# Performance work log

Measured on AMD Instinct MI355X. Metric: run time of the kernel, lower is better.

Reference implementation:

```python
import jax, jax.numpy as jnp
import numpy as np

NUM_LAYER = 5
EMB = 300
BN_EPS = 1e-5
NUM_BOND_TYPE = 6
NUM_BOND_DIR = 3
SELF_LOOP_TYPE = 4  # pretrain-gnns self-loop edge attr = [4, 0]


def setup_inputs() -> dict:
    key = jax.random.key(0)
    ks = jax.random.split(key, 12)
    N, E, D = 100000, 250000, EMB
    x = jax.random.normal(ks[0], (N, D), dtype=jnp.float32)
    edge_index = jax.random.randint(ks[1], (2, E), 0, N, dtype=jnp.int64)
    edge_attr = jax.random.randint(ks[2], (E, 2), 0, 3, dtype=jnp.int64)
    L = NUM_LAYER
    W1 = jax.random.normal(ks[3], (L, D, 2 * D), dtype=jnp.float32) * 0.05
    b1 = jnp.zeros((L, 2 * D), dtype=jnp.float32)
    W2 = jax.random.normal(ks[4], (L, 2 * D, D), dtype=jnp.float32) * 0.05
    b2 = jnp.zeros((L, D), dtype=jnp.float32)
    E1 = jax.random.normal(ks[5], (L, NUM_BOND_TYPE, D), dtype=jnp.float32) * 0.05
    E2 = jax.random.normal(ks[6], (L, NUM_BOND_DIR, D), dtype=jnp.float32) * 0.05
    gamma = jnp.ones((L, D), dtype=jnp.float32)
    beta = jnp.zeros((L, D), dtype=jnp.float32)
    return {"x": x, "edge_index": edge_index, "edge_attr": edge_attr,
            "W1": W1, "b1": b1, "W2": W2, "b2": b2,
            "E1": E1, "E2": E2, "gamma": gamma, "beta": beta}


def reference(x, edge_index, edge_attr, W1, b1, W2, b2, E1, E2, gamma, beta):
    N = x.shape[0]
    src, dst = edge_index[0], edge_index[1]
    bt, bd = edge_attr[:, 0], edge_attr[:, 1]
    h = x
    for l in range(NUM_LAYER):
        # GINEConv: message = x_j + edge_embedding, aggr='add', with self loops
        edge_emb = E1[l][bt] + E2[l][bd]                 # [E, D]
        self_emb = E1[l][SELF_LOOP_TYPE] + E2[l][0]      # [D]
        msg = h[src] + edge_emb                          # [E, D] gather
        agg = jax.ops.segment_sum(msg, dst, num_segments=N) + h + self_emb
        # update MLP: Linear(D,2D) -> ReLU -> Linear(2D,D)
        m = jax.nn.relu(agg @ W1[l] + b1[l]) @ W2[l] + b2[l]
        # BatchNorm1d in training mode (batch stats over nodes, biased var)
        mu = m.mean(axis=0)
        var = m.var(axis=0)
        m = (m - mu) * jax.lax.rsqrt(var + BN_EPS) * gamma[l] + beta[l]
        if l < NUM_LAYER - 1:  # ReLU on all but last layer; dropout ratio 0 -> no-op
            m = jax.nn.relu(m)
        h = m
    return h  # JK == 'last'
```

## Files before the change

kernel.cpp:

```cpp
#include <hip/hip_runtime.h>
#include <hip/hip_bf16.h>

#define NN 100000
#define NE 250000
#define DD 300
#define DDB 304
#define NL 5
#define MPAD 100096
#define KA1 320
#define N1 608
#define N1T 640
#define K2 608
#define N2T 384
#define NBLK 391
#define NCMB 19

typedef __attribute__((ext_vector_type(8))) short short8;
typedef __attribute__((ext_vector_type(4))) float f32x4;

#define GLBP(x) ((const __attribute__((address_space(1))) unsigned int*)(x))
#define LDSP(x) ((__attribute__((address_space(3))) unsigned int*)(x))
#define WAITV(N) asm volatile("s_waitcnt vmcnt(" #N ")" ::: "memory")

__device__ __forceinline__ ushort f2bf(float f){
  unsigned u = __float_as_uint(f);
  u += 0x7FFFu + ((u >> 16) & 1u);
  return (ushort)(u >> 16);
}
__device__ __forceinline__ float bf2f(ushort h){
  return __uint_as_float((unsigned)h << 16);
}
__device__ __forceinline__ unsigned pk2(float a, float b){
  return (unsigned)f2bf(a) | ((unsigned)f2bf(b) << 16);
}

__global__ void prep_weights(const float* __restrict__ W1, const float* __restrict__ W2,
                             ushort* __restrict__ W1T, ushort* __restrict__ W2T){
  int idx = blockIdx.x * 256 + threadIdx.x;
  const int total1 = NL * N1T * KA1;
  const int total2 = NL * N2T * K2;
  if (idx < total1){
    int l = idx / (N1T * KA1);
    int rem = idx % (N1T * KA1);
    int n = rem / KA1, k = rem % KA1;
    float v = (n < 2*DD && k < DD) ? W1[(size_t)l*DD*2*DD + (size_t)k*2*DD + n] : 0.0f;
    W1T[idx] = f2bf(v);
  } else {
    int idx2 = idx - total1;
    if (idx2 < total2){
      int l = idx2 / (N2T * K2);
      int rem = idx2 % (N2T * K2);
      int n = rem / K2, k = rem % K2;
      float v = (n < DD && k < 2*DD) ? W2[(size_t)l*2*DD*DD + (size_t)k*DD + n] : 0.0f;
      W2T[idx2] = f2bf(v);
    }
  }
}

__global__ void prep_ctab(const float* __restrict__ E1, const float* __restrict__ E2,
                          float* __restrict__ ctab){
  int idx = blockIdx.x * 256 + threadIdx.x;
  if (idx >= NL * NCMB * DDB) return;
  int l = idx / (NCMB * DDB);
  int rem = idx % (NCMB * DDB);
  int c = rem / DDB, d = rem % DDB;
  float v = 0.0f;
  if (d < DD){
    int bt = (c < 18) ? (c / 3) : 4;
    int bd = (c < 18) ? (c % 3) : 0;
    v = E1[(size_t)l*6*DD + bt*DD + d] + E2[(size_t)l*3*DD + bd*DD + d];
  }
  ctab[idx] = v;
}

__global__ void csr_count(const int* __restrict__ ei, int* __restrict__ deg){
  int e = blockIdx.x * 256 + threadIdx.x;
  if (e < NE) atomicAdd(&deg[ei[NE + e]], 1);
}

__global__ void scan_blk(const int* __restrict__ deg, int* __restrict__ rs, int* __restrict__ bsum){
  __shared__ int tmp[256];
  int i = blockIdx.x * 256 + threadIdx.x;
  int v = (i < NN) ? deg[i] : 0;
  tmp[threadIdx.x] = v;
  __syncthreads();
  #pragma unroll
  for (int off = 1; off < 256; off <<= 1){
    int t = (threadIdx.x >= off) ? tmp[threadIdx.x - off] : 0;
    __syncthreads();
    tmp[threadIdx.x] += t;
    __syncthreads();
  }
  if (i < NN) rs[i] = tmp[threadIdx.x] - v;
  if (threadIdx.x == 255) bsum[blockIdx.x] = tmp[255];
}

__global__ void scan_top(int* __restrict__ bsum){
  __shared__ int tmp[512];
  int v = (threadIdx.x < NBLK) ? bsum[threadIdx.x] : 0;
  tmp[threadIdx.x] = v;
  __syncthreads();
  #pragma unroll
  for (int off = 1; off < 512; off <<= 1){
    int t = (threadIdx.x >= off) ? tmp[threadIdx.x - off] : 0;
    __syncthreads();
    tmp[threadIdx.x] += t;
    __syncthreads();
  }
  if (threadIdx.x < NBLK) bsum[threadIdx.x] = tmp[threadIdx.x] - v;
}

__global__ void scan_add(int* __restrict__ rs, const int* __restrict__ bsum){
  int i = blockIdx.x * 256 + threadIdx.x;
  if (i < NN) rs[i] += bsum[blockIdx.x];
  if (i == 0) rs[NN] = NE;
}

__global__ void csr_fill(const int* __restrict__ ei, const int* __restrict__ ea,
                         const int* __restrict__ rs, int* __restrict__ cursor,
                         int* __restrict__ edges){
  int e = blockIdx.x * 256 + threadIdx.x;
  if (e < NE){
    int dst = ei[NE + e];
    int src = ei[e];
    int c = ea[2*e] * 3 + ea[2*e + 1];
    int p = rs[dst] + atomicAdd(&cursor[dst], 1);
    edges[p] = src | (c << 20);
  }
}

template<int HBF>
__global__ __launch_bounds__(256) void gather_agg(
    const void* __restrict__ hp, const float2* __restrict__ ss,
    const float* __restrict__ ctab_l,
    const int* __restrict__ rs, const int* __restrict__ edges,
    ushort* __restrict__ agg)
{
  int lane = threadIdx.x & 63;
  int wq = __builtin_amdgcn_readfirstlane(threadIdx.x >> 6);
  int wid = blockIdx.x * 4 + wq;
  int nw = gridDim.x * 4;
  int dA = lane * 4;
  int dB = 256 + lane * 4;
  bool laneB  = (lane < 16);
  bool validB = (dB < DD);

  float scA[4], shA[4], scB[4], shB[4];
  if (HBF){
    #pragma unroll
    for (int j = 0; j < 4; ++j){
      float2 s = ss[dA + j]; scA[j] = s.x; shA[j] = s.y;
    }
    if (validB){
      #pragma unroll
      for (int j = 0; j < 4; ++j){
        float2 s = ss[dB + j]; scB[j] = s.x; shB[j] = s.y;
      }
    }
  }

  const float*  hf = (const float*)hp;
  const ushort* hb = (const ushort*)hp;
  const float* ctS = ctab_l + 18*DDB;

  for (int row = wid; row < MPAD; row += nw){
    float a0=0,a1=0,a2=0,a3=0, b0=0,b1=0,b2=0,b3=0;
    if (row < NN){
      if (HBF){
        uint2 hw = *(const uint2*)(hb + (size_t)row*DDB + dA);
        a0 = fmaxf(bf2f((ushort)hw.x)*scA[0]+shA[0],0.f)      + ctS[dA+0];
        a1 = fmaxf(bf2f((ushort)(hw.x>>16))*scA[1]+shA[1],0.f)+ ctS[dA+1];
        a2 = fmaxf(bf2f((ushort)hw.y)*scA[2]+shA[2],0.f)      + ctS[dA+2];
        a3 = fmaxf(bf2f((ushort)(hw.y>>16))*scA[3]+shA[3],0.f)+ ctS[dA+3];
        if (validB){
          uint2 hv = *(const uint2*)(hb + (size_t)row*DDB + dB);
          b0 = fmaxf(bf2f((ushort)hv.x)*scB[0]+shB[0],0.f)      + ctS[dB+0];
          b1 = fmaxf(bf2f((ushort)(hv.x>>16))*scB[1]+shB[1],0.f)+ ctS[dB+1];
          b2 = fmaxf(bf2f((ushort)hv.y)*scB[2]+shB[2],0.f)      + ctS[dB+2];
          b3 = fmaxf(bf2f((ushort)(hv.y>>16))*scB[3]+shB[3],0.f)+ ctS[dB+3];
        }
      } else {
        float4 hv = *(const float4*)(hf + (size_t)row*DD + dA);
        a0 = hv.x + ctS[dA+0]; a1 = hv.y + ctS[dA+1];
        a2 = hv.z + ctS[dA+2]; a3 = hv.w + ctS[dA+3];
        if (validB){
          float4 hv2 = *(const float4*)(hf + (size_t)row*DD + dB);
          b0 = hv2.x + ctS[dB+0]; b1 = hv2.y + ctS[dB+1];
          b2 = hv2.z + ctS[dB+2]; b3 = hv2.w + ctS[dB+3];
        }
      }
      int p = rs[row], pe = rs[row + 1];
      for (; p < pe; ++p){
        int ew = edges[p];
        int src = ew & 0xFFFFF;
        const float* ct = ctab_l + (ew >> 20)*DDB;
        if (HBF){
          uint2 hw = *(const uint2*)(hb + (size_t)src*DDB + dA);
          a0 += fmaxf(bf2f((ushort)hw.x)*scA[0]+shA[0],0.f)      + ct[dA+0];
          a1 += fmaxf(bf2f((ushort)(hw.x>>16))*scA[1]+shA[1],0.f)+ ct[dA+1];
          a2 += fmaxf(bf2f((ushort)hw.y)*scA[2]+shA[2],0.f)      + ct[dA+2];
          a3 += fmaxf(bf2f((ushort)(hw.y>>16))*scA[3]+shA[3],0.f)+ ct[dA+3];
          if (validB){
            uint2 hv = *(const uint2*)(hb + (size_t)src*DDB + dB);
            b0 += fmaxf(bf2f((ushort)hv.x)*scB[0]+shB[0],0.f)      + ct[dB+0];
            b1 += fmaxf(bf2f((ushort)(hv.x>>16))*scB[1]+shB[1],0.f)+ ct[dB+1];
            b2 += fmaxf(bf2f((ushort)hv.y)*scB[2]+shB[2],0.f)      + ct[dB+2];
            b3 += fmaxf(bf2f((ushort)(hv.y>>16))*scB[3]+shB[3],0.f)+ ct[dB+3];
          }
        } else {
          float4 hv = *(const float4*)(hf + (size_t)src*DD + dA);
          a0 += hv.x + ct[dA+0]; a1 += hv.y + ct[dA+1];
          a2 += hv.z + ct[dA+2]; a3 += hv.w + ct[dA+3];
          if (validB){
            float4 hv2 = *(const float4*)(hf + (size_t)src*DD + dB);
            b0 += hv2.x + ct[dB+0]; b1 += hv2.y + ct[dB+1];
            b2 += hv2.z + ct[dB+2]; b3 += hv2.w + ct[dB+3];
          }
        }
      }
    }
    ushort* ag = agg + (size_t)row*KA1;
    uint2 oA; oA.x = pk2(a0, a1); oA.y = pk2(a2, a3);
    *(uint2*)(ag + dA) = oA;
    if (laneB){
      uint2 oB;
      if (validB){ oB.x = pk2(b0, b1); oB.y = pk2(b2, b3); }
      else       { oB.x = 0; oB.y = 0; }
      *(uint2*)(ag + dB) = oB;
    }
  }
}

template<int OUT_BF16, int RELU, int STATS>
__global__ __launch_bounds__(256) void gemm_128(
    const ushort* __restrict__ A, int lda,
    const ushort* __restrict__ B, int ldb,
    void* __restrict__ Cp, int ldc,
    int kTiles, const float* __restrict__ bias, int biasN,
    int Mvalid, int Nvalid, int nColTiles, float* __restrict__ statf)
{
  __shared__ ushort As[5][4096];
  __shared__ ushort Bs[5][4096];
  int tid = threadIdx.x;
  int lane = tid & 63, w = tid >> 6;
  int wm = (w >> 1) * 64, wn = (w & 1) * 64;

  int nwg = gridDim.x;
  int q = nwg >> 3, r = nwg & 7;
  int xcd = blockIdx.x & 7, idx = blockIdx.x >> 3;
  int bid = (xcd < r ? xcd * (q + 1) : r * (q + 1) + (xcd - r) * q) + idx;
  int m0 = (bid / nColTiles) * 128;
  int n0 = (bid % nColTiles) * 128;

  int r0 = tid >> 2;
  int kc = ((tid & 3) ^ ((tid >> 3) & 3)) * 8;
  const ushort* Ap = A + (size_t)(m0 + r0)*lda + kc;
  const ushort* Bp = B + (size_t)(n0 + r0)*ldb + kc;

  f32x4 acc[4][4] = {};

#define STAGE(buf, kt) do { \
    int _ko = (kt) * 32; \
    __builtin_amdgcn_global_load_lds(GLBP(Ap + _ko),                  LDSP(&As[buf][w*512]),        16, 0, 0); \
    __builtin_amdgcn_global_load_lds(GLBP(Ap + _ko + (size_t)64*lda), LDSP(&As[buf][w*512 + 2048]), 16, 0, 0); \
    __builtin_amdgcn_global_load_lds(GLBP(Bp + _ko),                  LDSP(&Bs[buf][w*512]),        16, 0, 0); \
    __builtin_amdgcn_global_load_lds(GLBP(Bp + _ko + (size_t)64*ldb), LDSP(&Bs[buf][w*512 + 2048]), 16, 0, 0); \
  } while (0)

  STAGE(0, 0); STAGE(1, 1); STAGE(2, 2); STAGE(3, 3);
  WAITV(12);
  __builtin_amdgcn_s_barrier();

  int fr = lane & 15;
  int ko8 = (((lane >> 4) ^ ((fr >> 1) & 3))) * 8;
  int cur = 0;
  for (int kt = 0; kt < kTiles; ++kt){
    int sb = cur + 4; if (sb >= 5) sb -= 5;
    if (kt + 4 < kTiles) STAGE(sb, kt + 4);
    short8 af[4], bfv[4];
    #pragma unroll
    for (int i = 0; i < 4; ++i)
      af[i] = *(const short8*)&As[cur][(wm + i*16 + fr)*32 + ko8];
    #pragma unroll
    for (int j = 0; j < 4; ++j)
      bfv[j] = *(const short8*)&Bs[cur][(wn + j*16 + fr)*32 + ko8];
    #pragma unroll
    for (int i = 0; i < 4; ++i)
      #pragma unroll
      for (int j = 0; j < 4; ++j)
        acc[i][j] = __builtin_amdgcn_mfma_f32_16x16x32_bf16(af[i], bfv[j], acc[i][j], 0, 0, 0);
    if (kt + 1 < kTiles){
      int rem = kTiles - kt;
      if      (rem >= 5) WAITV(12);
      else if (rem == 4) WAITV(8);
      else if (rem == 3) WAITV(4);
      else               WAITV(0);
      __builtin_amdgcn_s_barrier();
    }
    cur = cur + 1; if (cur >= 5) cur = 0;
  }
#undef STAGE

  int cc = lane & 15, cr = (lane >> 4) * 4;
  float ps[4], pq[4];
  if (STATS){
    #pragma unroll
    for (int j = 0; j < 4; ++j){ ps[j] = 0.0f; pq[j] = 0.0f; }
  }
  #pragma unroll
  for (int i = 0; i < 4; ++i){
    #pragma unroll
    for (int j = 0; j < 4; ++j){
      int col = n0 + wn + j*16 + cc;
      if (col >= Nvalid) continue;
      float bv = (col < biasN) ? bias[col] : 0.0f;
      #pragma unroll
      for (int r2 = 0; r2 < 4; ++r2){
        int row = m0 + wm + i*16 + cr + r2;
        if (row < Mvalid){
          float v = acc[i][j][r2] + bv;
          if (RELU) v = fmaxf(v, 0.0f);
          if (OUT_BF16) ((ushort*)Cp)[(size_t)row*ldc + col] = f2bf(v);
          else          ((float*) Cp)[(size_t)row*ldc + col] = v;
          if (STATS){ ps[j] += v; pq[j] += v * v; }
        }
      }
    }
  }
  if (STATS){
    #pragma unroll
    for (int j = 0; j < 4; ++j){
      float s = ps[j], qv = pq[j];
      s += __shfl_xor(s, 16); qv += __shfl_xor(qv, 16);
      s += __shfl_xor(s, 32); qv += __shfl_xor(qv, 32);
      int col = n0 + wn + j*16 + cc;
      if ((lane >> 4) == 0 && col < Nvalid){
        unsafeAtomicAdd(&statf[col], s);
        unsafeAtomicAdd(&statf[N2T + col], qv);
      }
    }
  }
}

template<int OUT_BF16, int RELU, int STATS>
__global__ __launch_bounds__(512) void gemm_256(
    const ushort* __restrict__ A, int lda,
    const ushort* __restrict__ B, int ldb,
    void* __restrict__ Cp, int ldc,
    int kTiles, const float* __restrict__ bias, int biasN,
    int Mvalid, int Nvalid, int nColTiles, float* __restrict__ statf)
{
  __shared__ ushort As[3][8192];
  __shared__ ushort Bs[3][4096];
  int tid = threadIdx.x;
  int lane = tid & 63, w = tid >> 6;
  int wm = (w >> 1) * 64, wn = (w & 1) * 64;

  int nwg = gridDim.x;
  int q = nwg >> 3, r = nwg & 7;
  int xcd = blockIdx.x & 7, idx = blockIdx.x >> 3;
  int bid = (xcd < r ? xcd * (q + 1) : r * (q + 1) + (xcd - r) * q) + idx;
  int m0 = (bid / nColTiles) * 256;
  int n0 = (bid % nColTiles) * 128;

  int r0 = tid >> 2;
  int kc = ((tid & 3) ^ ((tid >> 3) & 3)) * 8;
  const ushort* Ap = A + (size_t)(m0 + r0)*lda + kc;
  const ushort* Bp = B + (size_t)(n0 + r0)*ldb + kc;

  f32x4 acc[4][4] = {};

#define STAGE(buf, kt) do { \
    int _ko = (kt) * 32; \
    __builtin_amdgcn_global_load_lds(GLBP(Ap + _ko),                   LDSP(&As[buf][w*512]),        16, 0, 0); \
    __builtin_amdgcn_global_load_lds(GLBP(Ap + _ko + (size_t)128*lda), LDSP(&As[buf][w*512 + 4096]), 16, 0, 0); \
    __builtin_amdgcn_global_load_lds(GLBP(Bp + _ko),                   LDSP(&Bs[buf][w*512]),        16, 0, 0); \
  } while (0)

  STAGE(0, 0);
  STAGE(1, 1);
  WAITV(3);
  __builtin_amdgcn_s_barrier();

  int fr = lane & 15;
  int ko8 = (((lane >> 4) ^ ((fr >> 1) & 3))) * 8;
  int cur = 0;
  for (int kt = 0; kt < kTiles; ++kt){
    int sb = cur + 2; if (sb >= 3) sb -= 3;
    if (kt + 2 < kTiles) STAGE(sb, kt + 2);
    short8 af[4], bfv[4];
    #pragma unroll
    for (int i = 0; i < 4; ++i)
      af[i] = *(const short8*)&As[cur][(wm + i*16 + fr)*32 + ko8];
    #pragma unroll
    for (int j = 0; j < 4; ++j)
      bfv[j] = *(const short8*)&Bs[cur][(wn + j*16 + fr)*32 + ko8];
    #pragma unroll
    for (int i = 0; i < 4; ++i)
      #pragma unroll
      for (int j = 0; j < 4; ++j)
        acc[i][j] = __builtin_amdgcn_mfma_f32_16x16x32_bf16(af[i], bfv[j], acc[i][j], 0, 0, 0);
    if (kt + 1 < kTiles){
      if (kt + 2 < kTiles) WAITV(3);
      else                 WAITV(0);
      __builtin_amdgcn_s_barrier();
    }
    cur = cur + 1; if (cur >= 3) cur = 0;
  }
#undef STAGE

  int cc = lane & 15, cr = (lane >> 4) * 4;
  float ps[4], pq[4];
  if (STATS){
    #pragma unroll
    for (int j = 0; j < 4; ++j){ ps[j] = 0.0f; pq[j] = 0.0f; }
  }
  #pragma unroll
  for (int i = 0; i < 4; ++i){
    #pragma unroll
    for (int j = 0; j < 4; ++j){
      int col = n0 + wn + j*16 + cc;
      if (col >= Nvalid) continue;
      float bv = (col < biasN) ? bias[col] : 0.0f;
      #pragma unroll
      for (int r2 = 0; r2 < 4; ++r2){
        int row = m0 + wm + i*16 + cr + r2;
        if (row < Mvalid){
          float v = acc[i][j][r2] + bv;
          if (RELU) v = fmaxf(v, 0.0f);
          if (OUT_BF16) ((ushort*)Cp)[(size_t)row*ldc + col] = f2bf(v);
          else          ((float*) Cp)[(size_t)row*ldc + col] = v;
          if (STATS){ ps[j] += v; pq[j] += v * v; }
        }
      }
    }
  }
  if (STATS){
    #pragma unroll
    for (int j = 0; j < 4; ++j){
      float s = ps[j], qv = pq[j];
      s += __shfl_xor(s, 16); qv += __shfl_xor(qv, 16);
      s += __shfl_xor(s, 32); qv += __shfl_xor(qv, 32);
      int col = n0 + wn + j*16 + cc;
      if ((lane >> 4) == 0 && col < Nvalid){
        unsafeAtomicAdd(&statf[col], s);
        unsafeAtomicAdd(&statf[N2T + col], qv);
      }
    }
  }
}

__global__ void make_norm(const float* __restrict__ statf, const float* __restrict__ gamma,
                          const float* __restrict__ beta, float2* __restrict__ ss){
  int d = threadIdx.x;
  if (d >= DD) return;
  double mu = (double)statf[d] / (double)NN;
  double var = (double)statf[N2T + d] / (double)NN - mu * mu;
  float inv = rsqrtf((float)var + 1e-5f);
  float sc = inv * gamma[d];
  ss[d] = make_float2(sc, beta[d] - (float)mu * sc);
}

__global__ void apply_norm(const float* __restrict__ m2, const float2* __restrict__ ss,
                           float* __restrict__ out){
  int row = blockIdx.x;
  int d = threadIdx.x;
  if (d >= DD) return;
  float2 s = ss[d];
  out[(size_t)row*DD + d] = m2[(size_t)row*DD + d] * s.x + s.y;
}

extern "C" void kernel_launch(void* const* d_in, const int* in_sizes, int n_in,
                              void* d_out, int out_size, void* d_ws, size_t ws_size,
                              hipStream_t stream) {
  const float* x     = (const float*)d_in[0];
  const int*   ei    = (const int*)  d_in[1];
  const int*   ea    = (const int*)  d_in[2];
  const float* W1    = (const float*)d_in[3];
  const float* b1    = (const float*)d_in[4];
  const float* W2    = (const float*)d_in[5];
  const float* b2    = (const float*)d_in[6];
  const float* E1    = (const float*)d_in[7];
  const float* E2    = (const float*)d_in[8];
  const float* gamma = (const float*)d_in[9];
  const float* beta  = (const float*)d_in[10];

  char* p = (char*)d_ws;
  float*  m2buf = (float*) p; p += (size_t)NN * DD * 4;
  ushort* m2bf  = (ushort*)p; p += (size_t)NN * DDB * 2;
  ushort* agg   = (ushort*)p; p += (size_t)MPAD * KA1 * 2;
  ushort* m1    = (ushort*)p; p += (size_t)MPAD * N1 * 2;
  ushort* W1T   = (ushort*)p; p += (size_t)NL * N1T * KA1 * 2;
  ushort* W2T   = (ushort*)p; p += (size_t)NL * N2T * K2 * 2;
  float*  ctab  = (float*) p; p += (size_t)NL * NCMB * DDB * 4;
  int*    deg   = (int*)   p; p += (size_t)NN * 4;
  int*    rs    = (int*)   p; p += (size_t)(NN + 16) * 4;
  int*    bsum  = (int*)   p; p += (size_t)512 * 4;
  int*    cursor= (int*)   p; p += (size_t)NN * 4;
  int*    edges = (int*)   p; p += (size_t)NE * 4;
  float*  statf = (float*) p; p += (size_t)2 * N2T * 4;
  float2* ss    = (float2*)p;

  {
    int total = NL*N1T*KA1 + NL*N2T*K2;
    prep_weights<<<(total + 255)/256, 256, 0, stream>>>(W1, W2, W1T, W2T);
    int tc = NL * NCMB * DDB;
    prep_ctab<<<(tc + 255)/256, 256, 0, stream>>>(E1, E2, ctab);
  }
  hipMemsetAsync(deg, 0, (size_t)NN*4, stream);
  hipMemsetAsync(cursor, 0, (size_t)NN*4, stream);
  csr_count<<<(NE + 255)/256, 256, 0, stream>>>(ei, deg);
  scan_blk<<<NBLK, 256, 0, stream>>>(deg, rs, bsum);
  scan_top<<<1, 512, 0, stream>>>(bsum);
  scan_add<<<NBLK, 256, 0, stream>>>(rs, bsum);
  csr_fill<<<(NE + 255)/256, 256, 0, stream>>>(ei, ea, rs, cursor, edges);

  for (int l = 0; l < NL; ++l){
    const float* ctab_l = ctab + (size_t)l * NCMB * DDB;

    if (l == 0)
      gather_agg<0><<<2048, 256, 0, stream>>>(x, nullptr, ctab_l, rs, edges, agg);
    else
      gather_agg<1><<<2048, 256, 0, stream>>>(m2bf, ss, ctab_l, rs, edges, agg);

    gemm_128<1,1,0><<<(MPAD/128) * (N1T/128), 256, 0, stream>>>(
        agg, KA1, W1T + (size_t)l*N1T*KA1, KA1, m1, N1, KA1/32,
        b1 + (size_t)l*2*DD, 2*DD, MPAD, N1, N1T/128, nullptr);

    hipMemsetAsync(statf, 0, (size_t)2*N2T*4, stream);

    if (l < NL - 1)
      gemm_256<1,0,1><<<(MPAD/256) * (N2T/128), 512, 0, stream>>>(
          m1, N1, W2T + (size_t)l*N2T*K2, K2, m2bf, DDB, K2/32,
          b2 + (size_t)l*DD, DD, NN, DD, N2T/128, statf);
    else
      gemm_256<0,0,1><<<(MPAD/256) * (N2T/128), 512, 0, stream>>>(
          m1, N1, W2T + (size_t)l*N2T*K2, K2, m2buf, DD, K2/32,
          b2 + (size_t)l*DD, DD, NN, DD, N2T/128, statf);

    make_norm<<<1, 320, 0, stream>>>(statf, gamma + (size_t)l*DD, beta + (size_t)l*DD, ss);
  }
  apply_norm<<<NN, 320, 0, stream>>>(m2buf, ss, (float*)d_out);
}
```

Baseline: 1.753 ms.

## Use 256-row tiles for first GEMM, deepen second GEMM pipeline, XCD-chunk gather rows

The first MLP GEMM moves from a 128x128 tile with a 5-stage pipeline to a 256x128 tile with 512 threads and a 3-stage pipeline, which halves B-tile reloads per output row. The second GEMM gets a 4-stage prefetch pipeline instead of 3, using more LDS. The gather kernel now assigns each XCD a contiguous chunk of rows instead of striding across all of them, aiming to improve L2 locality per XCD. Risks are lower occupancy from the larger LDS footprint and load imbalance across chunks.

```diff
diff --git a/kernel.cpp b/kernel.cpp
--- a/kernel.cpp
+++ b/kernel.cpp
@@ -14,6 +14,7 @@
 #define N2T 384
 #define NBLK 391
 #define NCMB 19
+#define XCHUNK 12512
 
 typedef __attribute__((ext_vector_type(8))) short short8;
 typedef __attribute__((ext_vector_type(4))) float f32x4;
@@ -138,8 +139,11 @@
 {
   int lane = threadIdx.x & 63;
   int wq = __builtin_amdgcn_readfirstlane(threadIdx.x >> 6);
-  int wid = blockIdx.x * 4 + wq;
-  int nw = gridDim.x * 4;
+  int xcd  = blockIdx.x & 7;
+  int widx = (blockIdx.x >> 3) * 4 + wq;
+  int nwX  = (gridDim.x >> 3) * 4;
+  int rbeg = xcd * XCHUNK + widx;
+  int rend = (xcd + 1) * XCHUNK;
   int dA = lane * 4;
   int dB = 256 + lane * 4;
   bool laneB  = (lane < 16);
@@ -163,8 +167,8 @@
   const ushort* hb = (const ushort*)hp;
   const float* ctS = ctab_l + 18*DDB;
 
-  for (int row = wid; row < MPAD; row += nw){
-    float a0=0,a1=0,a2=0,a3=0, b0=0,b1=0,b2=0,b3=0;
+  for (int row = rbeg; row < rend; row += nwX){
+    float a0=0,a1=0,a2=0,a3=0, b0=0,b1v=0,b2v=0,b3=0;
     if (row < NN){
       if (HBF){
         uint2 hw = *(const uint2*)(hb + (size_t)row*DDB + dA);
@@ -174,10 +178,10 @@
         a3 = fmaxf(bf2f((ushort)(hw.y>>16))*scA[3]+shA[3],0.f)+ ctS[dA+3];
         if (validB){
           uint2 hv = *(const uint2*)(hb + (size_t)row*DDB + dB);
-          b0 = fmaxf(bf2f((ushort)hv.x)*scB[0]+shB[0],0.f)      + ctS[dB+0];
-          b1 = fmaxf(bf2f((ushort)(hv.x>>16))*scB[1]+shB[1],0.f)+ ctS[dB+1];
-          b2 = fmaxf(bf2f((ushort)hv.y)*scB[2]+shB[2],0.f)      + ctS[dB+2];
-          b3 = fmaxf(bf2f((ushort)(hv.y>>16))*scB[3]+shB[3],0.f)+ ctS[dB+3];
+          b0  = fmaxf(bf2f((ushort)hv.x)*scB[0]+shB[0],0.f)      + ctS[dB+0];
+          b1v = fmaxf(bf2f((ushort)(hv.x>>16))*scB[1]+shB[1],0.f)+ ctS[dB+1];
+          b2v = fmaxf(bf2f((ushort)hv.y)*scB[2]+shB[2],0.f)      + ctS[dB+2];
+          b3  = fmaxf(bf2f((ushort)(hv.y>>16))*scB[3]+shB[3],0.f)+ ctS[dB+3];
         }
       } else {
         float4 hv = *(const float4*)(hf + (size_t)row*DD + dA);
@@ -185,8 +189,8 @@
         a2 = hv.z + ctS[dA+2]; a3 = hv.w + ctS[dA+3];
         if (validB){
           float4 hv2 = *(const float4*)(hf + (size_t)row*DD + dB);
-          b0 = hv2.x + ctS[dB+0]; b1 = hv2.y + ctS[dB+1];
-          b2 = hv2.z + ctS[dB+2]; b3 = hv2.w + ctS[dB+3];
+          b0 = hv2.x + ctS[dB+0]; b1v = hv2.y + ctS[dB+1];
+          b2v = hv2.z + ctS[dB+2]; b3 = hv2.w + ctS[dB+3];
         }
       }
       int p = rs[row], pe = rs[row + 1];
@@ -202,10 +206,10 @@
           a3 += fmaxf(bf2f((ushort)(hw.y>>16))*scA[3]+shA[3],0.f)+ ct[dA+3];
           if (validB){
             uint2 hv = *(const uint2*)(hb + (size_t)src*DDB + dB);
-            b0 += fmaxf(bf2f((ushort)hv.x)*scB[0]+shB[0],0.f)      + ct[dB+0];
-            b1 += fmaxf(bf2f((ushort)(hv.x>>16))*scB[1]+shB[1],0.f)+ ct[dB+1];
-            b2 += fmaxf(bf2f((ushort)hv.y)*scB[2]+shB[2],0.f)      + ct[dB+2];
-            b3 += fmaxf(bf2f((ushort)(hv.y>>16))*scB[3]+shB[3],0.f)+ ct[dB+3];
+            b0  += fmaxf(bf2f((ushort)hv.x)*scB[0]+shB[0],0.f)      + ct[dB+0];
+            b1v += fmaxf(bf2f((ushort)(hv.x>>16))*scB[1]+shB[1],0.f)+ ct[dB+1];
+            b2v += fmaxf(bf2f((ushort)hv.y)*scB[2]+shB[2],0.f)      + ct[dB+2];
+            b3  += fmaxf(bf2f((ushort)(hv.y>>16))*scB[3]+shB[3],0.f)+ ct[dB+3];
           }
         } else {
           float4 hv = *(const float4*)(hf + (size_t)src*DD + dA);
@@ -213,8 +217,8 @@
           a2 += hv.z + ct[dA+2]; a3 += hv.w + ct[dA+3];
           if (validB){
             float4 hv2 = *(const float4*)(hf + (size_t)src*DD + dB);
-            b0 += hv2.x + ct[dB+0]; b1 += hv2.y + ct[dB+1];
-            b2 += hv2.z + ct[dB+2]; b3 += hv2.w + ct[dB+3];
+            b0 += hv2.x + ct[dB+0]; b1v += hv2.y + ct[dB+1];
+            b2v += hv2.z + ct[dB+2]; b3 += hv2.w + ct[dB+3];
           }
         }
       }
@@ -224,7 +228,7 @@
     *(uint2*)(ag + dA) = oA;
     if (laneB){
       uint2 oB;
-      if (validB){ oB.x = pk2(b0, b1); oB.y = pk2(b2, b3); }
+      if (validB){ oB.x = pk2(b0, b1v); oB.y = pk2(b2v, b3); }
       else       { oB.x = 0; oB.y = 0; }
       *(uint2*)(ag + dB) = oB;
     }
@@ -232,15 +236,15 @@
 }
 
 template<int OUT_BF16, int RELU, int STATS>
-__global__ __launch_bounds__(256) void gemm_128(
+__global__ __launch_bounds__(512) void gemm_256(
     const ushort* __restrict__ A, int lda,
     const ushort* __restrict__ B, int ldb,
     void* __restrict__ Cp, int ldc,
     int kTiles, const float* __restrict__ bias, int biasN,
     int Mvalid, int Nvalid, int nColTiles, float* __restrict__ statf)
 {
-  __shared__ ushort As[5][4096];
-  __shared__ ushort Bs[5][4096];
+  __shared__ ushort As[3][8192];
+  __shared__ ushort Bs[3][4096];
   int tid = threadIdx.x;
   int lane = tid & 63, w = tid >> 6;
   int wm = (w >> 1) * 64, wn = (w & 1) * 64;
@@ -249,7 +253,7 @@
   int q = nwg >> 3, r = nwg & 7;
   int xcd = blockIdx.x & 7, idx = blockIdx.x >> 3;
   int bid = (xcd < r ? xcd * (q + 1) : r * (q + 1) + (xcd - r) * q) + idx;
-  int m0 = (bid / nColTiles) * 128;
+  int m0 = (bid / nColTiles) * 256;
   int n0 = (bid % nColTiles) * 128;
 
   int r0 = tid >> 2;
@@ -261,22 +265,22 @@
 
 #define STAGE(buf, kt) do { \
     int _ko = (kt) * 32; \
-    __builtin_amdgcn_global_load_lds(GLBP(Ap + _ko),                  LDSP(&As[buf][w*512]),        16, 0, 0); \
-    __builtin_amdgcn_global_load_lds(GLBP(Ap + _ko + (size_t)64*lda), LDSP(&As[buf][w*512 + 2048]), 16, 0, 0); \
-    __builtin_amdgcn_global_load_lds(GLBP(Bp + _ko),                  LDSP(&Bs[buf][w*512]),        16, 0, 0); \
-    __builtin_amdgcn_global_load_lds(GLBP(Bp + _ko + (size_t)64*ldb), LDSP(&Bs[buf][w*512 + 2048]), 16, 0, 0); \
+    __builtin_amdgcn_global_load_lds(GLBP(Ap + _ko),                   LDSP(&As[buf][w*512]),        16, 0, 0); \
+    __builtin_amdgcn_global_load_lds(GLBP(Ap + _ko + (size_t)128*lda), LDSP(&As[buf][w*512 + 4096]), 16, 0, 0); \
+    __builtin_amdgcn_global_load_lds(GLBP(Bp + _ko),                   LDSP(&Bs[buf][w*512]),        16, 0, 0); \
   } while (0)
 
-  STAGE(0, 0); STAGE(1, 1); STAGE(2, 2); STAGE(3, 3);
-  WAITV(12);
+  STAGE(0, 0);
+  STAGE(1, 1);
+  WAITV(3);
   __builtin_amdgcn_s_barrier();
 
   int fr = lane & 15;
   int ko8 = (((lane >> 4) ^ ((fr >> 1) & 3))) * 8;
   int cur = 0;
   for (int kt = 0; kt < kTiles; ++kt){
-    int sb = cur + 4; if (sb >= 5) sb -= 5;
-    if (kt + 4 < kTiles) STAGE(sb, kt + 4);
+    int sb = cur + 2; if (sb >= 3) sb -= 3;
+    if (kt + 2 < kTiles) STAGE(sb, kt + 2);
     short8 af[4], bfv[4];
     #pragma unroll
     for (int i = 0; i < 4; ++i)
@@ -290,14 +294,11 @@
       for (int j = 0; j < 4; ++j)
         acc[i][j] = __builtin_amdgcn_mfma_f32_16x16x32_bf16(af[i], bfv[j], acc[i][j], 0, 0, 0);
     if (kt + 1 < kTiles){
-      int rem = kTiles - kt;
-      if      (rem >= 5) WAITV(12);
-      else if (rem == 4) WAITV(8);
-      else if (rem == 3) WAITV(4);
-      else               WAITV(0);
+      if (kt + 2 < kTiles) WAITV(3);
+      else                 WAITV(0);
       __builtin_amdgcn_s_barrier();
     }
-    cur = cur + 1; if (cur >= 5) cur = 0;
+    cur = cur + 1; if (cur >= 3) cur = 0;
   }
 #undef STAGE
 
@@ -343,15 +344,15 @@
 }
 
 template<int OUT_BF16, int RELU, int STATS>
-__global__ __launch_bounds__(512) void gemm_256(
+__global__ __launch_bounds__(512) void gemm_256_d3(
     const ushort* __restrict__ A, int lda,
     const ushort* __restrict__ B, int ldb,
     void* __restrict__ Cp, int ldc,
     int kTiles, const float* __restrict__ bias, int biasN,
     int Mvalid, int Nvalid, int nColTiles, float* __restrict__ statf)
 {
-  __shared__ ushort As[3][8192];
-  __shared__ ushort Bs[3][4096];
+  __shared__ ushort As[4][8192];
+  __shared__ ushort Bs[4][4096];
   int tid = threadIdx.x;
   int lane = tid & 63, w = tid >> 6;
   int wm = (w >> 1) * 64, wn = (w & 1) * 64;
@@ -379,15 +380,16 @@
 
   STAGE(0, 0);
   STAGE(1, 1);
-  WAITV(3);
+  STAGE(2, 2);
+  WAITV(6);
   __builtin_amdgcn_s_barrier();
 
   int fr = lane & 15;
   int ko8 = (((lane >> 4) ^ ((fr >> 1) & 3))) * 8;
   int cur = 0;
   for (int kt = 0; kt < kTiles; ++kt){
-    int sb = cur + 2; if (sb >= 3) sb -= 3;
-    if (kt + 2 < kTiles) STAGE(sb, kt + 2);
+    int sb = cur + 3; if (sb >= 4) sb -= 4;
+    if (kt + 3 < kTiles) STAGE(sb, kt + 3);
     short8 af[4], bfv[4];
     #pragma unroll
     for (int i = 0; i < 4; ++i)
@@ -401,11 +403,13 @@
       for (int j = 0; j < 4; ++j)
         acc[i][j] = __builtin_amdgcn_mfma_f32_16x16x32_bf16(af[i], bfv[j], acc[i][j], 0, 0, 0);
     if (kt + 1 < kTiles){
-      if (kt + 2 < kTiles) WAITV(3);
-      else                 WAITV(0);
+      int left = kTiles - 2 - kt;
+      if      (left >= 2) WAITV(6);
+      else if (left == 1) WAITV(3);
+      else                WAITV(0);
       __builtin_amdgcn_s_barrier();
     }
-    cur = cur + 1; if (cur >= 3) cur = 0;
+    cur = cur + 1; if (cur >= 4) cur = 0;
   }
 #undef STAGE
 
@@ -523,18 +527,18 @@
     else
       gather_agg<1><<<2048, 256, 0, stream>>>(m2bf, ss, ctab_l, rs, edges, agg);
 
-    gemm_128<1,1,0><<<(MPAD/128) * (N1T/128), 256, 0, stream>>>(
+    gemm_256<1,1,0><<<(MPAD/256) * (N1T/128), 512, 0, stream>>>(
         agg, KA1, W1T + (size_t)l*N1T*KA1, KA1, m1, N1, KA1/32,
         b1 + (size_t)l*2*DD, 2*DD, MPAD, N1, N1T/128, nullptr);
 
     hipMemsetAsync(statf, 0, (size_t)2*N2T*4, stream);
 
     if (l < NL - 1)
-      gemm_256<1,0,1><<<(MPAD/256) * (N2T/128), 512, 0, stream>>>(
+      gemm_256_d3<1,0,1><<<(MPAD/256) * (N2T/128), 512, 0, stream>>>(
           m1, N1, W2T + (size_t)l*N2T*K2, K2, m2bf, DDB, K2/32,
           b2 + (size_t)l*DD, DD, NN, DD, N2T/128, statf);
     else
-      gemm_256<0,0,1><<<(MPAD/256) * (N2T/128), 512, 0, stream>>>(
+      gemm_256_d3<0,0,1><<<(MPAD/256) * (N2T/128), 512, 0, stream>>>(
           m1, N1, W2T + (size_t)l*N2T*K2, K2, m2buf, DD, K2/32,
           b2 + (size_t)l*DD, DD, NN, DD, N2T/128, statf);
 
```

After: 1.722 ms. No clear change (-1.8%).
